# Kernel tuning notes

Hardware: AMD Instinct MI355X
Metric: run time of the kernel (lower is better)

The kernel has to match this reference:

```python
import jax, jax.numpy as jnp
import numpy as np

COUNT_PRIOR_LOG_ODDS = -2.0  # frozen value of exponential_decay(**cfg.OBJ_PRES_COUNT_LOG_PRIOR)
EPS = 1e-9                   # safe_log epsilon
B, H, W = 1024, 16, 16


def setup_inputs() -> dict:
    key = jax.random.key(0)
    k1, k2 = jax.random.split(key)
    z_pres = jax.random.uniform(k1, (B, 1, H, W), dtype=jnp.float32)
    z_pres_prob = jax.random.uniform(k2, (B, 1, H, W), dtype=jnp.float32)
    return {"z_pres": z_pres, "z_pres_prob": z_pres_prob}


def _safe_log(x):
    return jnp.log(x + EPS)


def reference(z_pres, z_pres_prob):
    b, _, h, w = z_pres.shape
    hw = h * w
    s = hw + 1  # count support size

    count_support = jnp.arange(s, dtype=jnp.float32)  # [S]
    p = 1.0 / (jnp.exp(jnp.float32(-COUNT_PRIOR_LOG_ODDS)) + 1.0)
    cd0 = (1.0 - p) * p ** count_support
    cd0 = cd0 / cd0.sum()
    cd0 = jnp.broadcast_to(cd0[None, :], (b, s))      # count_distribution [B, S]
    csf0 = jnp.zeros((b, 1), jnp.float32)             # count_so_far [B, 1]

    # flatten grid in row-major (h, w) order to scan axis: [HW, B, 1]
    probs = z_pres_prob.reshape(b, 1, hw).transpose(2, 0, 1)
    pres = z_pres.reshape(b, 1, hw).transpose(2, 0, 1)
    steps = jnp.arange(hw, dtype=jnp.float32)

    def step(carry, xs):
        cd, csf = carry                 # [B, S], [B, 1]
        prob, zp, i = xs                # [B, 1], [B, 1], scalar
        denom = hw - i
        # P(z=1 | C, z_prev): clamp(count_support - count_so_far, 0, HW - i) / (HW - i)
        p_z_given = jnp.clip(count_support[None, :] - csf, 0.0, denom) / denom  # [B, S]
        p_z = jnp.sum(cd * p_z_given, axis=1, keepdims=True)                    # [B, 1] (the bmm)
        kl = (prob * (_safe_log(prob) - _safe_log(p_z))
              + (1.0 - prob) * (_safe_log(1.0 - prob) - _safe_log(1.0 - p_z)))
        sample = jnp.round(zp)                                                  # [B, 1]
        mult = sample * p_z_given + (1.0 - sample) * (1.0 - p_z_given)          # [B, S]
        cd1 = mult * cd
        norm = jnp.clip(jnp.sum(cd1, axis=1, keepdims=True), 1e-6, None)
        return (cd1 / norm, csf + sample), kl

    (_, _), kls = jax.lax.scan(step, (cd0, csf0), (probs, pres, steps))
    # kls: [HW, B, 1] -> obj_kl [B, 1, H, W]
    return kls.transpose(1, 2, 0).reshape(b, 1, h, w)
```

## Files before the change

### kernel.cpp

```cpp
#include <hip/hip_runtime.h>
#include <math.h>

#define HW 256
#define MINNORM 1.17549435e-38f


template <int CTRL>
__device__ __forceinline__ float dpp_sra(float x) {
    int s = __builtin_amdgcn_update_dpp(0, __builtin_bit_cast(int, x),
                                        CTRL, 0xf, 0xf, true);
    return x + __builtin_bit_cast(float, s);
}

__device__ __forceinline__ float rdlane(float x, int l) {
    return __builtin_bit_cast(float,
        __builtin_amdgcn_readlane(__builtin_bit_cast(int, x), l));
}

__device__ __forceinline__ void wave_total2(float x, float y,
                                            float& sx, float& sy) {
    x = dpp_sra<0x111>(x);  y = dpp_sra<0x111>(y);
    x = dpp_sra<0x112>(x);  y = dpp_sra<0x112>(y);
    x = dpp_sra<0x114>(x);  y = dpp_sra<0x114>(y);
    x = dpp_sra<0x118>(x);  y = dpp_sra<0x118>(y);
    const float a0 = rdlane(x, 15), b0 = rdlane(y, 15);
    const float a1 = rdlane(x, 31), b1 = rdlane(y, 31);
    const float a2 = rdlane(x, 47), b2 = rdlane(y, 47);
    sx = (a0 + a1) + a2;
    sy = (b0 + b1) + b2;
}

__global__ void __launch_bounds__(64, 1)
spair_count_kl(const float* __restrict__ z_pres,
               const float* __restrict__ z_prob,
               float* __restrict__ out) {
    float tok;
    asm volatile("s_setreg_imm32_b32 hwreg(HW_REG_MODE, 4, 2), 0\n\t"
                 "v_mov_b32 %0, 0" : "=v"(tok));

    const int lane = threadIdx.x;
    const int b = blockIdx.x;

    const float e2f = (float)exp(2.0);
    const float pf  = (float)(1.0 / ((double)e2f + 1.0));
    const double pd = (double)pf;
    const double l2p = log2(pd);
    float cd = 0.0f;
    if (lane <= 41) {
        const double powj = exp2((double)lane * l2p);
        float v = (float)((1.0 - pd) * powj);
        cd = (v < MINNORM) ? 0.0f : v;
    }
    {
        float s = cd;
#pragma unroll
        for (int off = 32; off > 0; off >>= 1) s += __shfl_xor(s, off, 64);
        cd = cd / s;
    }
    cd += tok;
    const float jf = (float)lane;
    float csf = tok;

    const float it0 = 1.0f / (float)(HW - lane);
    const float it1 = 1.0f / (float)(HW - 64 - lane);
    const float it2 = 1.0f / (float)(HW - 128 - lane);
    const float it3 = 1.0f / (float)(HW - 192 - lane);

    const float* presb = z_pres + (size_t)b * HW;
    const float* probb = z_prob + (size_t)b * HW;
    float* outb = out + (size_t)b * HW;

    bool dead = false;

#pragma unroll 1
    for (int k = 0; k < 4; ++k) {
        const float myprob = probb[k * 64 + lane];
        const float mypres = presb[k * 64 + lane];
        const unsigned long long smask = __ballot(rintf(mypres) != 0.0f);
        float my_pz = 0.0f;
        const float itk = (k == 0) ? it0 : (k == 1) ? it1 : (k == 2) ? it2 : it3;

        if (!dead) {
#pragma unroll 1
            for (int blk = 0; blk < 4; ++blk) {
                float p2 = 1.0f;
#pragma unroll
                for (int u = 0; u < 16; ++u) {
                    const int ii = blk * 16 + u;
                    const int i = k * 64 + ii;
                    const float fden = (float)(HW - i);
                    const float inv = rdlane(itk, ii);
                    const bool s1 = ((smask >> ii) & 1ULL) != 0ULL;

                    const float t = fminf(fmaxf(jf - csf, 0.0f), fden);
                    const float pg = (t == fden) ? 1.0f : t * inv;
                    const float mult = s1 ? pg : (1.0f - pg);

                    const float prodm = cd * mult;
                    const float p1 = cd * pg;
                    float p1s;
                    wave_total2(prodm, p1, p2, p1s);
                    const float norm = fmaxf(p2, 1e-6f);
                    const float invn = __builtin_amdgcn_rcpf(norm);
                    cd = prodm * invn;
                    csf += s1 ? 1.0f : 0.0f;

                    const float pz = s1 ? p2 : p1s;
                    my_pz = (ii == lane) ? pz : my_pz;
                }
                if (p2 == 0.0f) { dead = true; break; }
            }
        }

        const float prob = myprob;
        const float pz = my_pz;
        const float kl = prob * (logf(prob + 1e-9f) - logf(pz + 1e-9f))
                       + (1.0f - prob) * (logf((1.0f - prob) + 1e-9f)
                                        - logf((1.0f - pz) + 1e-9f));
        outb[k * 64 + lane] = kl;
    }
}

extern "C" void kernel_launch(void* const* d_in, const int* in_sizes, int n_in,
                              void* d_out, int out_size, void* d_ws, size_t ws_size,
                              hipStream_t stream) {
    const float* z_pres = (const float*)d_in[0];
    const float* z_prob = (const float*)d_in[1];
    float* out = (float*)d_out;
    const int nbatch = in_sizes[0] / HW;
    spair_count_kl<<<dim3(nbatch), dim3(64), 0, stream>>>(z_pres, z_prob, out);
}
```

Before: 70.15 us.

## Pack four batch rows per wavefront using 16-lane DPP row reductions

Each 64-lane wavefront now handles four batch elements, one per 16-lane row. Each lane holds three count-support entries, and the per-step sum uses row-local DPP adds instead of cross-row readlanes. Inverse denominators move to shared memory and sample values are read as float4 loads instead of a ballot mask. This removes the serial readlane chain and cuts the grid to a quarter of the wavefronts, but adds per-lane work per step, drops the clamp logic that covered support values up to 41 (now 47), and makes early exit wait until all four rows are dead.

```diff
diff --git a/kernel.cpp b/kernel.cpp
--- a/kernel.cpp
+++ b/kernel.cpp
@@ -6,28 +6,19 @@
 
 
 template <int CTRL>
-__device__ __forceinline__ float dpp_sra(float x) {
+__device__ __forceinline__ float dpp_add(float x) {
     int s = __builtin_amdgcn_update_dpp(0, __builtin_bit_cast(int, x),
                                         CTRL, 0xf, 0xf, true);
     return x + __builtin_bit_cast(float, s);
 }
 
-__device__ __forceinline__ float rdlane(float x, int l) {
-    return __builtin_bit_cast(float,
-        __builtin_amdgcn_readlane(__builtin_bit_cast(int, x), l));
-}
-
-__device__ __forceinline__ void wave_total2(float x, float y,
-                                            float& sx, float& sy) {
-    x = dpp_sra<0x111>(x);  y = dpp_sra<0x111>(y);
-    x = dpp_sra<0x112>(x);  y = dpp_sra<0x112>(y);
-    x = dpp_sra<0x114>(x);  y = dpp_sra<0x114>(y);
-    x = dpp_sra<0x118>(x);  y = dpp_sra<0x118>(y);
-    const float a0 = rdlane(x, 15), b0 = rdlane(y, 15);
-    const float a1 = rdlane(x, 31), b1 = rdlane(y, 31);
-    const float a2 = rdlane(x, 47), b2 = rdlane(y, 47);
-    sx = (a0 + a1) + a2;
-    sy = (b0 + b1) + b2;
+__device__ __forceinline__ void row_total2(float x, float y,
+                                           float& sx, float& sy) {
+    x = dpp_add<0xB1>(x);   y = dpp_add<0xB1>(y);
+    x = dpp_add<0x4E>(x);   y = dpp_add<0x4E>(y);
+    x = dpp_add<0x128>(x);  y = dpp_add<0x128>(y);
+    x = dpp_add<0x124>(x);  y = dpp_add<0x124>(y);
+    sx = x; sy = y;
 }
 
 __global__ void __launch_bounds__(64, 1)
@@ -38,33 +29,42 @@
     asm volatile("s_setreg_imm32_b32 hwreg(HW_REG_MODE, 4, 2), 0\n\t"
                  "v_mov_b32 %0, 0" : "=v"(tok));
 
+    __shared__ float invt[HW];
+
     const int lane = threadIdx.x;
-    const int b = blockIdx.x;
+    const int l16  = lane & 15;
+    const int row  = lane >> 4;
+    const int b    = blockIdx.x * 4 + row;
+
+#pragma unroll
+    for (int i = 0; i < 4; ++i)
+        invt[i * 64 + lane] = 1.0f / (float)(HW - (i * 64 + lane));
+    __syncthreads();
 
     const float e2f = (float)exp(2.0);
     const float pf  = (float)(1.0 / ((double)e2f + 1.0));
     const double pd = (double)pf;
     const double l2p = log2(pd);
-    float cd = 0.0f;
-    if (lane <= 41) {
-        const double powj = exp2((double)lane * l2p);
-        float v = (float)((1.0 - pd) * powj);
-        cd = (v < MINNORM) ? 0.0f : v;
+    float cd0, cd1, cd2;
+    {
+        float c[3];
+#pragma unroll
+        for (int sl = 0; sl < 3; ++sl) {
+            const int j = sl * 16 + l16;
+            const double powj = exp2((double)j * l2p);
+            float v = (float)((1.0 - pd) * powj);
+            c[sl] = (v < MINNORM) ? 0.0f : v;
+        }
+        float ssum = (c[0] + c[1]) + c[2];
+        ssum = dpp_add<0xB1>(ssum);  ssum = dpp_add<0x4E>(ssum);
+        ssum = dpp_add<0x128>(ssum); ssum = dpp_add<0x124>(ssum);
+        cd0 = c[0] / ssum; cd1 = c[1] / ssum; cd2 = c[2] / ssum;
     }
-    {
-        float s = cd;
-#pragma unroll
-        for (int off = 32; off > 0; off >>= 1) s += __shfl_xor(s, off, 64);
-        cd = cd / s;
-    }
-    cd += tok;
-    const float jf = (float)lane;
+    cd0 += tok; cd1 += tok; cd2 += tok;
     float csf = tok;
-
-    const float it0 = 1.0f / (float)(HW - lane);
-    const float it1 = 1.0f / (float)(HW - 64 - lane);
-    const float it2 = 1.0f / (float)(HW - 128 - lane);
-    const float it3 = 1.0f / (float)(HW - 192 - lane);
+    const float jf0 = (float)l16;
+    const float jf1 = (float)(16 + l16);
+    const float jf2 = (float)(32 + l16);
 
     const float* presb = z_pres + (size_t)b * HW;
     const float* probb = z_prob + (size_t)b * HW;
@@ -73,51 +73,58 @@
     bool dead = false;
 
 #pragma unroll 1
-    for (int k = 0; k < 4; ++k) {
-        const float myprob = probb[k * 64 + lane];
-        const float mypres = presb[k * 64 + lane];
-        const unsigned long long smask = __ballot(rintf(mypres) != 0.0f);
-        float my_pz = 0.0f;
-        const float itk = (k == 0) ? it0 : (k == 1) ? it1 : (k == 2) ? it2 : it3;
+    for (int k = 0; k < 16; ++k) {
+        float mypz = 0.0f;
+        float p2last = 0.0f;
+        if (!dead) {
+#pragma unroll
+            for (int c4 = 0; c4 < 4; ++c4) {
+                const float4 zp4 = *reinterpret_cast<const float4*>(presb + k * 16 + c4 * 4);
+                const float4 iv4 = *reinterpret_cast<const float4*>(&invt[k * 16 + c4 * 4]);
+#pragma unroll
+                for (int u = 0; u < 4; ++u) {
+                    const int ii = c4 * 4 + u;
+                    const float zp  = (u == 0) ? zp4.x : (u == 1) ? zp4.y
+                                    : (u == 2) ? zp4.z : zp4.w;
+                    const float inv = (u == 0) ? iv4.x : (u == 1) ? iv4.y
+                                    : (u == 2) ? iv4.z : iv4.w;
 
-        if (!dead) {
-#pragma unroll 1
-            for (int blk = 0; blk < 4; ++blk) {
-                float p2 = 1.0f;
-#pragma unroll
-                for (int u = 0; u < 16; ++u) {
-                    const int ii = blk * 16 + u;
-                    const int i = k * 64 + ii;
-                    const float fden = (float)(HW - i);
-                    const float inv = rdlane(itk, ii);
-                    const bool s1 = ((smask >> ii) & 1ULL) != 0ULL;
+                    const float s    = rintf(zp);
+                    const float sgn  = fmaf(s, 2.0f, -1.0f);
+                    const float base = 1.0f - s;
 
-                    const float t = fminf(fmaxf(jf - csf, 0.0f), fden);
-                    const float pg = (t == fden) ? 1.0f : t * inv;
-                    const float mult = s1 ? pg : (1.0f - pg);
+                    const float t0 = jf0 - csf, t1 = jf1 - csf, t2 = jf2 - csf;
+                    const float pg0 = t0 * inv, pg1 = t1 * inv, pg2 = t2 * inv;
 
-                    const float prodm = cd * mult;
-                    const float p1 = cd * pg;
-                    float p1s;
-                    wave_total2(prodm, p1, p2, p1s);
+                    const float m0 = fmaf(pg0, sgn, base);
+                    const float m1 = fmaf(pg1, sgn, base);
+                    const float m2 = fmaf(pg2, sgn, base);
+
+                    const float pr0 = cd0 * m0, pr1 = cd1 * m1, pr2 = cd2 * m2;
+                    const float y0 = cd0 * pg0, y1 = cd1 * pg1, y2 = cd2 * pg2;
+
+                    float p2, p1s;
+                    row_total2((pr0 + pr1) + pr2, (y0 + y1) + y2, p2, p1s);
+
                     const float norm = fmaxf(p2, 1e-6f);
                     const float invn = __builtin_amdgcn_rcpf(norm);
-                    cd = prodm * invn;
-                    csf += s1 ? 1.0f : 0.0f;
+                    cd0 = pr0 * invn; cd1 = pr1 * invn; cd2 = pr2 * invn;
+                    csf += s;
 
-                    const float pz = s1 ? p2 : p1s;
-                    my_pz = (ii == lane) ? pz : my_pz;
+                    const float pz = (s != 0.0f) ? p2 : p1s;
+                    mypz = (l16 == ii) ? pz : mypz;
+                    p2last = p2;
                 }
-                if (p2 == 0.0f) { dead = true; break; }
             }
+            if (__ballot(p2last != 0.0f) == 0ULL) dead = true;
         }
 
-        const float prob = myprob;
-        const float pz = my_pz;
+        const float prob = probb[k * 16 + l16];
+        const float pz = mypz;
         const float kl = prob * (logf(prob + 1e-9f) - logf(pz + 1e-9f))
                        + (1.0f - prob) * (logf((1.0f - prob) + 1e-9f)
                                         - logf((1.0f - pz) + 1e-9f));
-        outb[k * 64 + lane] = kl;
+        outb[k * 16 + l16] = kl;
     }
 }
 
@@ -128,5 +135,5 @@
     const float* z_prob = (const float*)d_in[1];
     float* out = (float*)d_out;
     const int nbatch = in_sizes[0] / HW;
-    spair_count_kl<<<dim3(nbatch), dim3(64), 0, stream>>>(z_pres, z_prob, out);
+    spair_count_kl<<<dim3(nbatch / 4), dim3(64), 0, stream>>>(z_pres, z_prob, out);
 }
```

After: 67.68 us. -3.5%, faster.
